# Kernel optimization log

Measured on AMD Instinct MI355X. Metric: run time of the kernel, lower is better.

The kernel has to match this reference:

```python
import jax, jax.numpy as jnp
import numpy as np

H = 1024      # hidden_size
NH = 16       # num_heads
HD = H // NH  # head_dim


def setup_inputs() -> dict:
    key = jax.random.key(0)
    ks = jax.random.split(key, 5)
    x = jax.random.normal(ks[0], (2, 2048, H), dtype=jnp.float32)
    # nn.Linear weights are [out, in]; keep that convention
    w_qkv = jax.random.normal(ks[1], (3 * H, H), dtype=jnp.float32) * (1.0 / np.sqrt(H))
    b_qkv = jax.random.normal(ks[2], (3 * H,), dtype=jnp.float32) * 0.01
    w_out = jax.random.normal(ks[3], (H, H), dtype=jnp.float32) * (1.0 / np.sqrt(H))
    b_out = jax.random.normal(ks[4], (H,), dtype=jnp.float32) * 0.01
    return {"x": x, "w_qkv": w_qkv, "b_qkv": b_qkv, "w_out": w_out, "b_out": b_out}


def reference(x, w_qkv, b_qkv, w_out, b_out):
    B, L, _ = x.shape
    scale = HD ** -0.5
    qkv = x @ w_qkv.T + b_qkv                       # [B,L,3H]
    qkv = qkv.reshape(B, L, 3, NH, HD).transpose(2, 0, 3, 1, 4)  # [3,B,NH,L,HD]
    q, k, v = qkv[0], qkv[1], qkv[2]
    attn = jnp.einsum('bhqd,bhkd->bhqk', q, k) * scale
    attn = jax.nn.softmax(attn, axis=-1)            # dropout is identity in eval
    out = jnp.einsum('bhqk,bhkd->bhqd', attn, v)    # [B,NH,L,HD]
    out = out.transpose(0, 2, 1, 3).reshape(B, L, H)
    return out @ w_out.T + b_out
```

## Files before the change

### kernel.cpp

```cpp
#include <hip/hip_runtime.h>
#include <hip/hip_bf16.h>
#include <stdint.h>

#define H_DIM  1024
#define NHEADS 16
#define HDIM   64
#define BATCH  2
#define SEQ    2048
#define MROWS  (BATCH * SEQ)
#define QKV_N  (3 * H_DIM)
#define QK_LD  (2 * H_DIM)
#define NT     (SEQ / 64)

typedef __attribute__((ext_vector_type(8))) __bf16 bf16x8;
typedef __attribute__((ext_vector_type(4))) float  floatx4;

__device__ __forceinline__ unsigned short f2bf(float f) {
    uint32_t u = __float_as_uint(f);
    u += 0x7fffu + ((u >> 16) & 1u);
    return (unsigned short)(u >> 16);
}
__device__ __forceinline__ float bf2f(unsigned short u) {
    return __uint_as_float(((uint32_t)u) << 16);
}
__device__ __forceinline__ uint32_t cvtpk_bf16(float lo, float hi) {
    uint32_t r;
    asm("v_cvt_pk_bf16_f32 %0, %1, %2" : "=v"(r) : "v"(lo), "v"(hi));
    return r;
}

#if __has_builtin(__builtin_amdgcn_exp2f)
#define fexp2 __builtin_amdgcn_exp2f
#else
#define fexp2 exp2f
#endif

__device__ __forceinline__ void async_ld16(const void* g, void* l) {
    __builtin_amdgcn_global_load_lds(
        (const __attribute__((address_space(1))) void*)g,
        (__attribute__((address_space(3))) void*)l, 16, 0, 0);
}

#define N4_X   (MROWS * H_DIM / 4)
#define N4_WQ  (QKV_N * H_DIM / 4)
#define N4_WO  (H_DIM * H_DIM / 4)
#define N4_TOT (N4_X + N4_WQ + N4_WO)
__global__ __launch_bounds__(256) void cvt_all(const float4* __restrict__ x,
                                               const float4* __restrict__ wq,
                                               const float4* __restrict__ wo,
                                               ushort4* __restrict__ xb,
                                               ushort4* __restrict__ wqb,
                                               ushort4* __restrict__ wob) {
    for (int i = blockIdx.x * 256 + threadIdx.x; i < N4_TOT; i += gridDim.x * 256) {
        const float4* in;
        ushort4* out;
        int j;
        if (i < N4_X)                { in = x;  out = xb;  j = i; }
        else if (i < N4_X + N4_WQ)   { in = wq; out = wqb; j = i - N4_X; }
        else                         { in = wo; out = wob; j = i - N4_X - N4_WQ; }
        float4 v = in[j];
        ushort4 o;
        o.x = f2bf(v.x); o.y = f2bf(v.y); o.z = f2bf(v.z); o.w = f2bf(v.w);
        out[j] = o;
    }
}

__global__ __launch_bounds__(256) void transpose_v(const unsigned short* __restrict__ vr,
                                                   unsigned short* __restrict__ vt) {
    __shared__ unsigned short T[64][72];
    const int tid = threadIdx.x;
    const int bh = blockIdx.y;
    const int b = bh >> 4, h = bh & 15;
    const int kv0 = blockIdx.x * 64;
    const int r  = tid >> 2, cs = (tid & 3) * 16;

    const unsigned short* src = &vr[(size_t)(b * SEQ + kv0 + r) * H_DIM + h * HDIM + cs];
    union { uint4 q; unsigned short u[8]; } A0, A1;
    A0.q = *(const uint4*)&src[0];
    A1.q = *(const uint4*)&src[8];
    #pragma unroll
    for (int e = 0; e < 8; ++e) T[cs + e][r]     = A0.u[e];
    #pragma unroll
    for (int e = 0; e < 8; ++e) T[cs + 8 + e][r] = A1.u[e];
    __syncthreads();

    const int dd = tid >> 2, ks = (tid & 3) * 16;
    unsigned short* dst = &vt[((size_t)bh * HDIM + dd) * SEQ + kv0 + ks];
    *(uint4*)&dst[0] = *(const uint4*)&T[dd][ks];
    *(uint4*)&dst[8] = *(const uint4*)&T[dd][ks + 8];
}

__global__ __launch_bounds__(256) void gemm_bt(const unsigned short* __restrict__ A,
                                               const unsigned short* __restrict__ B,
                                               const float* __restrict__ bias,
                                               unsigned short* __restrict__ Cb,
                                               float* __restrict__ Cf,
                                               unsigned short* __restrict__ Vr,
                                               int ldc, int Kdim) {
    __shared__ __align__(16) unsigned short As2[2][128 * 32];
    __shared__ __align__(16) unsigned short Bs2[2][128 * 32];
    const int tid  = threadIdx.x;
    const int lane = tid & 63;
    const int wave = tid >> 6;
    const int waveM = (wave >> 1) * 64;
    const int waveN = (wave & 1) * 64;

    const int nwg = gridDim.x * gridDim.y;
    int wg = blockIdx.y * gridDim.x + blockIdx.x;
    wg = (wg & 7) * (nwg >> 3) + (wg >> 3);
    const int bm = wg / gridDim.x, bn = wg % gridDim.x;

    floatx4 acc[4][4];
    #pragma unroll
    for (int i = 0; i < 4; ++i)
        #pragma unroll
        for (int j = 0; j < 4; ++j) {
            floatx4 z = {0.f, 0.f, 0.f, 0.f};
            acc[i][j] = z;
        }

    const unsigned short* pA[2];
    const unsigned short* pB[2];
    #pragma unroll
    for (int i = 0; i < 2; ++i) {
        int c = i * 256 + tid;
        int row = c >> 2;
        int kc  = (((c & 3) ^ (row & 3) ^ ((row >> 2) & 3))) * 8;
        pA[i] = A + (size_t)(bm * 128 + row) * Kdim + kc;
        pB[i] = B + (size_t)(bn * 128 + row) * Kdim + kc;
    }

    const int lr = lane & 15;
    const int g  = lane >> 4;
    const int pgx = (lr & 3) ^ ((lr >> 2) & 3);

    #define STAGEG(bi)                                                  \
        {                                                               \
            _Pragma("unroll")                                           \
            for (int i = 0; i < 2; ++i) {                               \
                async_ld16(pA[i], (char*)As2[bi] + i * 4096 + wave * 1024); \
                async_ld16(pB[i], (char*)Bs2[bi] + i * 4096 + wave * 1024); \
                pA[i] += 32; pB[i] += 32;                               \
            }                                                           \
        }

    STAGEG(0)

    int buf = 0;
    const int nst = Kdim / 32;
    for (int st = 0; st < nst; ++st) {
        if (st + 1 < nst) {
            STAGEG(buf ^ 1)
            asm volatile("s_waitcnt vmcnt(4)" ::: "memory");
        } else {
            asm volatile("s_waitcnt vmcnt(0)" ::: "memory");
        }
        __builtin_amdgcn_s_barrier();

        const int gk = (g ^ pgx) * 8;
        bf16x8 af[4], bfr[4];
        #pragma unroll
        for (int i = 0; i < 4; ++i)
            af[i] = *(const bf16x8*)&As2[buf][(waveM + i * 16 + lr) * 32 + gk];
        #pragma unroll
        for (int j = 0; j < 4; ++j)
            bfr[j] = *(const bf16x8*)&Bs2[buf][(waveN + j * 16 + lr) * 32 + gk];

        #pragma unroll
        for (int i = 0; i < 4; ++i)
            #pragma unroll
            for (int j = 0; j < 4; ++j)
                acc[i][j] = __builtin_amdgcn_mfma_f32_16x16x32_bf16(af[i], bfr[j], acc[i][j], 0, 0, 0);

        __builtin_amdgcn_s_barrier();
        buf ^= 1;
    }
    #undef STAGEG

    const int crow0 = bm * 128 + waveM + (lane >> 4) * 4;
    const int ccol0 = bn * 128 + waveN + (lane & 15);
    #pragma unroll
    for (int i = 0; i < 4; ++i)
        #pragma unroll
        for (int j = 0; j < 4; ++j) {
            int col = ccol0 + j * 16;
            float bv = bias[col];
            #pragma unroll
            for (int r = 0; r < 4; ++r) {
                int row = crow0 + i * 16 + r;
                float v = acc[i][j][r] + bv;
                if (Vr && col >= 2 * H_DIM) {
                    Vr[(size_t)row * H_DIM + (col - 2 * H_DIM)] = f2bf(v);
                } else if (Cb) {
                    Cb[(size_t)row * ldc + col] = f2bf(v);
                } else {
                    Cf[(size_t)row * ldc + col] = v;
                }
            }
        }
}

__global__ __launch_bounds__(256) void gemm_bt64(const unsigned short* __restrict__ A,
                                                 const unsigned short* __restrict__ B,
                                                 const float* __restrict__ bias,
                                                 float* __restrict__ Cf,
                                                 int ldc, int Kdim) {
    __shared__ __align__(16) unsigned short As[128 * 64];
    __shared__ __align__(16) unsigned short Bs[64 * 64];
    const int tid  = threadIdx.x;
    const int lane = tid & 63;
    const int wave = tid >> 6;
    const int waveM = wave * 32;

    const int nwg = gridDim.x * gridDim.y;
    int wg = blockIdx.y * gridDim.x + blockIdx.x;
    wg = (wg & 7) * (nwg >> 3) + (wg >> 3);
    const int bm = wg / gridDim.x, bn = wg % gridDim.x;

    floatx4 acc[2][4];
    #pragma unroll
    for (int i = 0; i < 2; ++i)
        #pragma unroll
        for (int j = 0; j < 4; ++j) {
            floatx4 z = {0.f, 0.f, 0.f, 0.f};
            acc[i][j] = z;
        }

    const unsigned short* pA[4];
    const unsigned short* pB[2];
    #pragma unroll
    for (int i = 0; i < 4; ++i) {
        int c = i * 256 + tid;
        int row = c >> 3;
        int kc  = ((c & 7) ^ (row & 7)) * 8;
        pA[i] = A + (size_t)(bm * 128 + row) * Kdim + kc;
        if (i < 2) pB[i] = B + (size_t)(bn * 64 + row) * Kdim + kc;
    }

    const int lr = lane & 15;
    const int g  = lane >> 4;
    const int sw = lr & 7;

    for (int k0 = 0; k0 < Kdim; k0 += 64) {
        #pragma unroll
        for (int i = 0; i < 4; ++i) {
            async_ld16(pA[i], (char*)As + i * 4096 + wave * 1024);
            pA[i] += 64;
        }
        #pragma unroll
        for (int i = 0; i < 2; ++i) {
            async_ld16(pB[i], (char*)Bs + i * 4096 + wave * 1024);
            pB[i] += 64;
        }
        __syncthreads();

        #pragma unroll
        for (int kk = 0; kk < 2; ++kk) {
            const int gk = (((kk << 2) + g) ^ sw) * 8;
            bf16x8 af[2], bfr[4];
            #pragma unroll
            for (int i = 0; i < 2; ++i)
                af[i] = *(const bf16x8*)&As[(waveM + i * 16 + lr) * 64 + gk];
            #pragma unroll
            for (int j = 0; j < 4; ++j)
                bfr[j] = *(const bf16x8*)&Bs[(j * 16 + lr) * 64 + gk];

            #pragma unroll
            for (int i = 0; i < 2; ++i)
                #pragma unroll
                for (int j = 0; j < 4; ++j)
                    acc[i][j] = __builtin_amdgcn_mfma_f32_16x16x32_bf16(af[i], bfr[j], acc[i][j], 0, 0, 0);
        }
        __syncthreads();
    }

    const int crow0 = bm * 128 + waveM + (lane >> 4) * 4;
    const int ccol0 = bn * 64 + (lane & 15);
    #pragma unroll
    for (int i = 0; i < 2; ++i)
        #pragma unroll
        for (int j = 0; j < 4; ++j) {
            int col = ccol0 + j * 16;
            float bv = bias[col];
            #pragma unroll
            for (int r = 0; r < 4; ++r) {
                int row = crow0 + i * 16 + r;
                Cf[(size_t)row * ldc + col] = acc[i][j][r] + bv;
            }
        }
}

__global__ __launch_bounds__(256, 2) void attn_mfma(const unsigned short* __restrict__ qkv2,
                                                    const unsigned short* __restrict__ vt,
                                                    unsigned short* __restrict__ ctx) {
    __shared__ __align__(16) unsigned short Ks2[2][64 * 64];
    __shared__ __align__(16) unsigned short Vt2[2][64 * 64];

    const int tid  = threadIdx.x;
    const int lane = tid & 63;
    const int wave = tid >> 6;

    const int f  = blockIdx.y * gridDim.x + blockIdx.x;
    const int bh = ((f >> 7) << 3) + (f & 7);
    const int qt = (f >> 3) & 15;
    const int b  = bh >> 4, h = bh & 15;
    const int q0 = qt * 128 + wave * 32;
    const int lq = lane & 15;
    const int g  = lane >> 4;
    const int swz = lq & 7;

    const float QS = 0.125f * 1.44269504f;
    bf16x8 qf[2][2];
    #pragma unroll
    for (int s = 0; s < 2; ++s)
        #pragma unroll
        for (int kk = 0; kk < 2; ++kk) {
            union { bf16x8 v; unsigned short u[8]; } tq;
            tq.v = *(const bf16x8*)&qkv2[(size_t)(b * SEQ + q0 + s * 16 + lq) * QK_LD
                                         + h * HDIM + kk * 32 + g * 8];
            #pragma unroll
            for (int e = 0; e < 8; ++e) tq.u[e] = f2bf(bf2f(tq.u[e]) * QS);
            qf[s][kk] = tq.v;
        }

    floatx4 acc_o[2][4];
    #pragma unroll
    for (int s = 0; s < 2; ++s)
        #pragma unroll
        for (int j = 0; j < 4; ++j) {
            floatx4 z = {0.f, 0.f, 0.f, 0.f};
            acc_o[s][j] = z;
        }
    float l_run[2] = {0.f, 0.f};

    const unsigned short* gK = qkv2 + (size_t)b * SEQ * QK_LD + H_DIM + (size_t)h * HDIM;
    const unsigned short* gV = vt + (size_t)bh * HDIM * SEQ;

    const int r0  = tid >> 3;
    const int pr0 = (r0 & 32) | ((r0 & 12) << 1) | ((r0 & 16) >> 2) | (r0 & 3);
    const int gs0 = (tid & 7) ^ (r0 & 7);
    const unsigned short* pK0 = gK + (size_t)pr0 * QK_LD + gs0 * 8;
    const unsigned short* pK1 = gK + (size_t)(pr0 + 32) * QK_LD + gs0 * 8;
    const unsigned short* pV0 = gV + (size_t)r0 * SEQ + gs0 * 8;
    const unsigned short* pV1 = gV + (size_t)(r0 + 32) * SEQ + gs0 * 8;

    #define STAGE_KV(bi)                                                        \
        {                                                                       \
            async_ld16(pK0, (char*)&Ks2[bi][0] + (wave * 64) * 16);             \
            async_ld16(pK1, (char*)&Ks2[bi][0] + (256 + wave * 64) * 16);       \
            async_ld16(pV0, (char*)&Vt2[bi][0] + (wave * 64) * 16);             \
            async_ld16(pV1, (char*)&Vt2[bi][0] + (256 + wave * 64) * 16);       \
            pK0 += 64 * QK_LD; pK1 += 64 * QK_LD; pV0 += 64; pV1 += 64;         \
        }

    STAGE_KV(0)
    __syncthreads();

    int buf = 0;
    for (int t = 0; t < NT; ++t) {
        if (t + 1 < NT) STAGE_KV(buf ^ 1)

        const unsigned short* Ksb = &Ks2[buf][0];
        const unsigned short* Vsb = &Vt2[buf][0];

        bf16x8 kf[4][2];
        #pragma unroll
        for (int jb = 0; jb < 4; ++jb)
            #pragma unroll
            for (int kk = 0; kk < 2; ++kk)
                kf[jb][kk] = *(const bf16x8*)&Ksb[(jb * 16 + lq) * 64 + (((kk << 2) + g) ^ swz) * 8];

        bf16x8 vf[4][2];
        #pragma unroll
        for (int dt = 0; dt < 4; ++dt)
            #pragma unroll
            for (int kk = 0; kk < 2; ++kk)
                vf[dt][kk] = *(const bf16x8*)&Vsb[(dt * 16 + lq) * 64 + (((kk << 2) + g) ^ swz) * 8];

        __builtin_amdgcn_sched_barrier(0);

        floatx4 sa[2][4];
        #pragma unroll
        for (int s = 0; s < 2; ++s)
            #pragma unroll
            for (int jb = 0; jb < 4; ++jb) {
                floatx4 z = {0.f, 0.f, 0.f, 0.f};
                sa[s][jb] = z;
            }
        __builtin_amdgcn_s_setprio(1);
        #pragma unroll
        for (int s = 0; s < 2; ++s)
            #pragma unroll
            for (int jb = 0; jb < 4; ++jb)
                #pragma unroll
                for (int kk = 0; kk < 2; ++kk)
                    sa[s][jb] = __builtin_amdgcn_mfma_f32_16x16x32_bf16(kf[jb][kk], qf[s][kk], sa[s][jb], 0, 0, 0);
        __builtin_amdgcn_s_setprio(0);

        #pragma unroll
        for (int s = 0; s < 2; ++s) {
            float ps = 0.f;
            {
                float e00 = fexp2(sa[s][0][0]), e01 = fexp2(sa[s][0][1]), e02 = fexp2(sa[s][0][2]), e03 = fexp2(sa[s][0][3]);
                float e10 = fexp2(sa[s][1][0]), e11 = fexp2(sa[s][1][1]), e12 = fexp2(sa[s][1][2]), e13 = fexp2(sa[s][1][3]);
                ps += ((e00 + e01) + (e02 + e03)) + ((e10 + e11) + (e12 + e13));
                union { bf16x8 v; uint32_t u[4]; } pf;
                pf.u[0] = cvtpk_bf16(e00, e01); pf.u[1] = cvtpk_bf16(e02, e03);
                pf.u[2] = cvtpk_bf16(e10, e11); pf.u[3] = cvtpk_bf16(e12, e13);
                __builtin_amdgcn_s_setprio(1);
                #pragma unroll
                for (int dt = 0; dt < 4; ++dt)
                    acc_o[s][dt] = __builtin_amdgcn_mfma_f32_16x16x32_bf16(pf.v, vf[dt][0], acc_o[s][dt], 0, 0, 0);
                __builtin_amdgcn_s_setprio(0);
            }
            {
                float e00 = fexp2(sa[s][2][0]), e01 = fexp2(sa[s][2][1]), e02 = fexp2(sa[s][2][2]), e03 = fexp2(sa[s][2][3]);
                float e10 = fexp2(sa[s][3][0]), e11 = fexp2(sa[s][3][1]), e12 = fexp2(sa[s][3][2]), e13 = fexp2(sa[s][3][3]);
                ps += ((e00 + e01) + (e02 + e03)) + ((e10 + e11) + (e12 + e13));
                union { bf16x8 v; uint32_t u[4]; } pf;
                pf.u[0] = cvtpk_bf16(e00, e01); pf.u[1] = cvtpk_bf16(e02, e03);
                pf.u[2] = cvtpk_bf16(e10, e11); pf.u[3] = cvtpk_bf16(e12, e13);
                __builtin_amdgcn_s_setprio(1);
                #pragma unroll
                for (int dt = 0; dt < 4; ++dt)
                    acc_o[s][dt] = __builtin_amdgcn_mfma_f32_16x16x32_bf16(pf.v, vf[dt][1], acc_o[s][dt], 0, 0, 0);
                __builtin_amdgcn_s_setprio(0);
            }
            ps += __shfl_xor(ps, 16);
            ps += __shfl_xor(ps, 32);
            l_run[s] += ps;
        }

        __syncthreads();
        buf ^= 1;
    }
    #undef STAGE_KV

    #pragma unroll
    for (int s = 0; s < 2; ++s) {
        float linv[4];
        #pragma unroll
        for (int r = 0; r < 4; ++r)
            linv[r] = 1.f / __shfl(l_run[s], g * 4 + r);
        #pragma unroll
        for (int dt = 0; dt < 4; ++dt)
            #pragma unroll
            for (int r = 0; r < 4; ++r)
                ctx[(size_t)(b * SEQ + q0 + s * 16 + g * 4 + r) * H_DIM + h * HDIM + dt * 16 + lq]
                    = f2bf(acc_o[s][dt][r] * linv[r]);
    }
}

extern "C" void kernel_launch(void* const* d_in, const int* in_sizes, int n_in,
                              void* d_out, int out_size, void* d_ws, size_t ws_size,
                              hipStream_t stream) {
    const float* x     = (const float*)d_in[0];
    const float* w_qkv = (const float*)d_in[1];
    const float* b_qkv = (const float*)d_in[2];
    const float* w_out = (const float*)d_in[3];
    const float* b_out = (const float*)d_in[4];
    float* out = (float*)d_out;

    unsigned short* xb    = (unsigned short*)d_ws;
    unsigned short* wqkvb = xb    + (size_t)MROWS * H_DIM;
    unsigned short* woutb = wqkvb + (size_t)QKV_N * H_DIM;
    unsigned short* qkv2  = woutb + (size_t)H_DIM * H_DIM;
    unsigned short* ctxb  = qkv2  + (size_t)MROWS * QK_LD;
    unsigned short* vtb   = ctxb  + (size_t)MROWS * H_DIM;
    unsigned short* vrows = ctxb;

    cvt_all<<<2048, 256, 0, stream>>>(
        (const float4*)x, (const float4*)w_qkv, (const float4*)w_out,
        (ushort4*)xb, (ushort4*)wqkvb, (ushort4*)woutb);

    gemm_bt<<<dim3(QKV_N / 128, MROWS / 128), 256, 0, stream>>>(
        xb, wqkvb, b_qkv, qkv2, nullptr, vrows, QK_LD, H_DIM);

    transpose_v<<<dim3(SEQ / 64, BATCH * NHEADS), 256, 0, stream>>>(vrows, vtb);

    attn_mfma<<<dim3(SEQ / 128, BATCH * NHEADS), 256, 0, stream>>>(qkv2, vtb, ctxb);

    gemm_bt64<<<dim3(H_DIM / 64, MROWS / 128), 256, 0, stream>>>(
        ctxb, woutb, b_out, out, H_DIM, H_DIM);
}
```

Before: 185.7 us.

## Double-buffer out-projection GEMM and use partial vmcnt waits in attention

The 64-wide GEMM kernel now double-buffers its A/B shared-memory tiles, issuing the next K-slab's async loads before computing on the current one. Both it and the attention kernel replace __syncthreads with explicit s_waitcnt vmcnt(N) plus raw s_barrier, so only the older buffer's loads must land before compute. This overlaps global-to-LDS transfer with MFMA work. It doubles GEMM LDS usage, which may reduce occupancy, and it relies on hand-counted vmcnt values matching the async loads each thread issues.

```diff
diff --git a/kernel.cpp b/kernel.cpp
--- a/kernel.cpp
+++ b/kernel.cpp
@@ -205,8 +205,8 @@
                                                  const float* __restrict__ bias,
                                                  float* __restrict__ Cf,
                                                  int ldc, int Kdim) {
-    __shared__ __align__(16) unsigned short As[128 * 64];
-    __shared__ __align__(16) unsigned short Bs[64 * 64];
+    __shared__ __align__(16) unsigned short As2[2][128 * 64];
+    __shared__ __align__(16) unsigned short Bs2[2][64 * 64];
     const int tid  = threadIdx.x;
     const int lane = tid & 63;
     const int wave = tid >> 6;
@@ -241,18 +241,32 @@
     const int g  = lane >> 4;
     const int sw = lr & 7;
 
-    for (int k0 = 0; k0 < Kdim; k0 += 64) {
-        #pragma unroll
-        for (int i = 0; i < 4; ++i) {
-            async_ld16(pA[i], (char*)As + i * 4096 + wave * 1024);
-            pA[i] += 64;
-        }
-        #pragma unroll
-        for (int i = 0; i < 2; ++i) {
-            async_ld16(pB[i], (char*)Bs + i * 4096 + wave * 1024);
-            pB[i] += 64;
-        }
-        __syncthreads();
+    #define STAGE64(bi)                                                         \
+        {                                                                       \
+            _Pragma("unroll")                                                   \
+            for (int i = 0; i < 4; ++i) {                                       \
+                async_ld16(pA[i], (char*)As2[bi] + i * 4096 + wave * 1024);     \
+                pA[i] += 64;                                                    \
+            }                                                                   \
+            _Pragma("unroll")                                                   \
+            for (int i = 0; i < 2; ++i) {                                       \
+                async_ld16(pB[i], (char*)Bs2[bi] + i * 4096 + wave * 1024);     \
+                pB[i] += 64;                                                    \
+            }                                                                   \
+        }
+
+    STAGE64(0)
+
+    int buf = 0;
+    const int nit = Kdim / 64;
+    for (int it = 0; it < nit; ++it) {
+        if (it + 1 < nit) {
+            STAGE64(buf ^ 1)
+            asm volatile("s_waitcnt vmcnt(6)" ::: "memory");
+        } else {
+            asm volatile("s_waitcnt vmcnt(0)" ::: "memory");
+        }
+        __builtin_amdgcn_s_barrier();
 
         #pragma unroll
         for (int kk = 0; kk < 2; ++kk) {
@@ -260,10 +274,10 @@
             bf16x8 af[2], bfr[4];
             #pragma unroll
             for (int i = 0; i < 2; ++i)
-                af[i] = *(const bf16x8*)&As[(waveM + i * 16 + lr) * 64 + gk];
+                af[i] = *(const bf16x8*)&As2[buf][(waveM + i * 16 + lr) * 64 + gk];
             #pragma unroll
             for (int j = 0; j < 4; ++j)
-                bfr[j] = *(const bf16x8*)&Bs[(j * 16 + lr) * 64 + gk];
+                bfr[j] = *(const bf16x8*)&Bs2[buf][(j * 16 + lr) * 64 + gk];
 
             #pragma unroll
             for (int i = 0; i < 2; ++i)
@@ -271,8 +285,10 @@
                 for (int j = 0; j < 4; ++j)
                     acc[i][j] = __builtin_amdgcn_mfma_f32_16x16x32_bf16(af[i], bfr[j], acc[i][j], 0, 0, 0);
         }
-        __syncthreads();
-    }
+        __builtin_amdgcn_s_barrier();
+        buf ^= 1;
+    }
+    #undef STAGE64
 
     const int crow0 = bm * 128 + waveM + (lane >> 4) * 4;
     const int ccol0 = bn * 64 + (lane & 15);
@@ -354,11 +370,16 @@
         }
 
     STAGE_KV(0)
-    __syncthreads();
 
     int buf = 0;
     for (int t = 0; t < NT; ++t) {
-        if (t + 1 < NT) STAGE_KV(buf ^ 1)
+        if (t + 1 < NT) {
+            STAGE_KV(buf ^ 1)
+            asm volatile("s_waitcnt vmcnt(4)" ::: "memory");
+        } else {
+            asm volatile("s_waitcnt vmcnt(0)" ::: "memory");
+        }
+        __builtin_amdgcn_s_barrier();
 
         const unsigned short* Ksb = &Ks2[buf][0];
         const unsigned short* Vsb = &Vt2[buf][0];
@@ -431,7 +452,7 @@
             l_run[s] += ps;
         }
 
-        __syncthreads();
+        __builtin_amdgcn_s_barrier();
         buf ^= 1;
     }
     #undef STAGE_KV
```

Measured after the change: 181.2 us. 2.4% less time.
